# Optimization experiments

Hardware: AMD Instinct MI355X
Metric: run time of the kernel (lower is better)

## Reference

```python
import jax, jax.numpy as jnp
import numpy as np

SOBEL_X = jnp.array([[-1., 0., 1.], [-2., 0., 2.], [-1., 0., 1.]], dtype=jnp.float32).reshape(1, 1, 3, 3)
SOBEL_Y = jnp.array([[-1., -2., -1.], [0., 0., 0.], [1., 2., 1.]], dtype=jnp.float32).reshape(1, 1, 3, 3)


def _gray(x):
    # x: (B, 3, H, W) -> (B, 1, H, W)
    if x.shape[1] == 3:
        return 0.299 * x[:, 0:1] + 0.587 * x[:, 1:2] + 0.114 * x[:, 2:3]
    return x


def _edges(g):
    # g: (B, 1, H, W); 3x3 Sobel convs with padding 1 (cross-correlation, like torch conv2d)
    dn = ('NCHW', 'OIHW', 'NCHW')
    ex = jax.lax.conv_general_dilated(g, SOBEL_X, (1, 1), ((1, 1), (1, 1)), dimension_numbers=dn)
    ey = jax.lax.conv_general_dilated(g, SOBEL_Y, (1, 1), ((1, 1), (1, 1)), dimension_numbers=dn)
    return jnp.sqrt(ex * ex + ey * ey)


def setup_inputs() -> dict:
    key = jax.random.key(0)
    k1, k2 = jax.random.split(key)
    pred = jax.random.normal(k1, (32, 3, 512, 512), dtype=jnp.float32)
    target = jax.random.normal(k2, (32, 3, 512, 512), dtype=jnp.float32)
    return {"pred": pred, "target": target}


def reference(pred, target):
    pred_edges = _edges(_gray(pred))
    target_edges = _edges(_gray(target))
    return jnp.mean(jnp.abs(pred_edges - target_edges))
```

## Files before the change

### kernel.cpp

```cpp
#include <hip/hip_runtime.h>


#define BATCH 32
#define HH 512
#define WW 512
#define IMG ((size_t)HH * WW)
#define CHUNKS 128
#define TOTAL (BATCH * HH * CHUNKS)
#define GRID 2048

__global__ void zero_out_kernel(float* out) { out[0] = 0.0f; }

__device__ __forceinline__ float gray1(float r, float g, float b) {
    return 0.299f * r + 0.587f * g + 0.114f * b;
}

#define MAG(a0, a1, a2, b0, b2, c0, c1, c2)                              \
    ({ float ex_ = ((a2) - (a0)) + 2.0f * ((b2) - (b0)) + ((c2) - (c0)); \
       float ey_ = ((c0) - (a0)) + 2.0f * ((c1) - (a1)) + ((c2) - (a2)); \
       sqrtf(ex_ * ex_ + ey_ * ey_); })

__device__ __forceinline__ void edges4(const float* __restrict__ base,
                                       int row, int x0, bool okl, bool okr,
                                       float e[4])
{
    float g[3][6];
    #pragma unroll
    for (int k = 0; k < 3; ++k) {
        const int gy = row - 1 + k;
        if ((unsigned)gy < (unsigned)HH) {
            const float* rbase = base + (size_t)gy * WW;
            const float4 mr = *(const float4*)(rbase + x0);
            const float4 mg = *(const float4*)(rbase + IMG + x0);
            const float4 mb = *(const float4*)(rbase + 2 * IMG + x0);
            float lr = 0.f, lg = 0.f, lb = 0.f;
            float rr = 0.f, rg = 0.f, rb = 0.f;
            if (okl) {
                lr = rbase[x0 - 1];
                lg = rbase[IMG + x0 - 1];
                lb = rbase[2 * IMG + x0 - 1];
            }
            if (okr) {
                rr = rbase[x0 + 4];
                rg = rbase[IMG + x0 + 4];
                rb = rbase[2 * IMG + x0 + 4];
            }
            g[k][0] = gray1(lr, lg, lb);
            g[k][1] = gray1(mr.x, mg.x, mb.x);
            g[k][2] = gray1(mr.y, mg.y, mb.y);
            g[k][3] = gray1(mr.z, mg.z, mb.z);
            g[k][4] = gray1(mr.w, mg.w, mb.w);
            g[k][5] = gray1(rr, rg, rb);
        } else {
            #pragma unroll
            for (int i = 0; i < 6; ++i) g[k][i] = 0.f;
        }
    }
    #pragma unroll
    for (int j = 0; j < 4; ++j)
        e[j] = MAG(g[0][j], g[0][j + 1], g[0][j + 2],
                   g[1][j],             g[1][j + 2],
                   g[2][j], g[2][j + 1], g[2][j + 2]);
}

__global__ __launch_bounds__(256, 4) void edge_loss_kernel(
    const float* __restrict__ pred,
    const float* __restrict__ target,
    float* __restrict__ out)
{
    const int tid = threadIdx.x;
    float lsum = 0.0f;

    for (int idx = blockIdx.x * 256 + tid; idx < TOTAL; idx += GRID * 256) {
        const int img   = idx >> 16;
        const int row   = (idx >> 7) & 511;
        const int chunk = idx & 127;
        const int x0    = chunk << 2;
        const bool okl  = (chunk > 0);
        const bool okr  = (chunk < CHUNKS - 1);

        const float* pb = pred   + (size_t)img * 3 * IMG;
        const float* tb = target + (size_t)img * 3 * IMG;

        float ep[4], et[4];
        edges4(pb, row, x0, okl, okr, ep);
        edges4(tb, row, x0, okl, okr, et);

        lsum += fabsf(ep[0] - et[0]) + fabsf(ep[1] - et[1])
              + fabsf(ep[2] - et[2]) + fabsf(ep[3] - et[3]);
    }

    #pragma unroll
    for (int off = 32; off > 0; off >>= 1)
        lsum += __shfl_down(lsum, off, 64);

    __shared__ float wsum[4];
    const int lane = tid & 63;
    const int wav  = tid >> 6;
    if (lane == 0) wsum[wav] = lsum;
    __syncthreads();
    if (tid == 0) {
        const float s = wsum[0] + wsum[1] + wsum[2] + wsum[3];
        const float inv_n = 1.0f / ((float)BATCH * HH * WW);
        atomicAdd(out, s * inv_n);
    }
}

extern "C" void kernel_launch(void* const* d_in, const int* in_sizes, int n_in,
                              void* d_out, int out_size, void* d_ws, size_t ws_size,
                              hipStream_t stream) {
    const float* pred   = (const float*)d_in[0];
    const float* target = (const float*)d_in[1];
    float* out = (float*)d_out;

    zero_out_kernel<<<1, 1, 0, stream>>>(out);

    edge_loss_kernel<<<dim3(GRID, 1, 1), 256, 0, stream>>>(pred, target, out);
}
```

Before: 268.9 us.

## Use row-per-wave sliding window with lane shuffles for Sobel halos

```diff
diff --git a/kernel.cpp b/kernel.cpp
--- a/kernel.cpp
+++ b/kernel.cpp
@@ -5,104 +5,131 @@
 #define HH 512
 #define WW 512
 #define IMG ((size_t)HH * WW)
-#define CHUNKS 128
-#define TOTAL (BATCH * HH * CHUNKS)
-#define GRID 2048
 
 __global__ void zero_out_kernel(float* out) { out[0] = 0.0f; }
-
-__device__ __forceinline__ float gray1(float r, float g, float b) {
-    return 0.299f * r + 0.587f * g + 0.114f * b;
-}
 
 #define MAG(a0, a1, a2, b0, b2, c0, c1, c2)                              \
     ({ float ex_ = ((a2) - (a0)) + 2.0f * ((b2) - (b0)) + ((c2) - (c0)); \
        float ey_ = ((c0) - (a0)) + 2.0f * ((c1) - (a1)) + ((c2) - (a2)); \
        sqrtf(ex_ * ex_ + ey_ * ey_); })
 
-__device__ __forceinline__ void edges4(const float* __restrict__ base,
-                                       int row, int x0, bool okl, bool okr,
-                                       float e[4])
-{
-    float g[3][6];
-    #pragma unroll
-    for (int k = 0; k < 3; ++k) {
-        const int gy = row - 1 + k;
-        if ((unsigned)gy < (unsigned)HH) {
-            const float* rbase = base + (size_t)gy * WW;
-            const float4 mr = *(const float4*)(rbase + x0);
-            const float4 mg = *(const float4*)(rbase + IMG + x0);
-            const float4 mb = *(const float4*)(rbase + 2 * IMG + x0);
-            float lr = 0.f, lg = 0.f, lb = 0.f;
-            float rr = 0.f, rg = 0.f, rb = 0.f;
-            if (okl) {
-                lr = rbase[x0 - 1];
-                lg = rbase[IMG + x0 - 1];
-                lb = rbase[2 * IMG + x0 - 1];
-            }
-            if (okr) {
-                rr = rbase[x0 + 4];
-                rg = rbase[IMG + x0 + 4];
-                rb = rbase[2 * IMG + x0 + 4];
-            }
-            g[k][0] = gray1(lr, lg, lb);
-            g[k][1] = gray1(mr.x, mg.x, mb.x);
-            g[k][2] = gray1(mr.y, mg.y, mb.y);
-            g[k][3] = gray1(mr.z, mg.z, mb.z);
-            g[k][4] = gray1(mr.w, mg.w, mb.w);
-            g[k][5] = gray1(rr, rg, rb);
-        } else {
-            #pragma unroll
-            for (int i = 0; i < 6; ++i) g[k][i] = 0.f;
-        }
-    }
-    #pragma unroll
-    for (int j = 0; j < 4; ++j)
-        e[j] = MAG(g[0][j], g[0][j + 1], g[0][j + 2],
-                   g[1][j],             g[1][j + 2],
-                   g[2][j], g[2][j + 1], g[2][j + 2]);
-}
+#define LG(R, gy_) do {                                                   \
+    const int gy__ = (gy_);                                               \
+    if ((unsigned)gy__ < (unsigned)HH) {                                  \
+        const float* rp__ = pb + (size_t)gy__ * WW + cx;                  \
+        float4 x0_ = *(const float4*)(rp__);                              \
+        float4 x1_ = *(const float4*)(rp__ + 4);                          \
+        float4 y0_ = *(const float4*)(rp__ + IMG);                        \
+        float4 y1_ = *(const float4*)(rp__ + IMG + 4);                    \
+        float4 z0_ = *(const float4*)(rp__ + 2 * IMG);                    \
+        float4 z1_ = *(const float4*)(rp__ + 2 * IMG + 4);                \
+        R##p0 = 0.299f * x0_.x + 0.587f * y0_.x + 0.114f * z0_.x;         \
+        R##p1 = 0.299f * x0_.y + 0.587f * y0_.y + 0.114f * z0_.y;         \
+        R##p2 = 0.299f * x0_.z + 0.587f * y0_.z + 0.114f * z0_.z;         \
+        R##p3 = 0.299f * x0_.w + 0.587f * y0_.w + 0.114f * z0_.w;         \
+        R##p4 = 0.299f * x1_.x + 0.587f * y1_.x + 0.114f * z1_.x;         \
+        R##p5 = 0.299f * x1_.y + 0.587f * y1_.y + 0.114f * z1_.y;         \
+        R##p6 = 0.299f * x1_.z + 0.587f * y1_.z + 0.114f * z1_.z;         \
+        R##p7 = 0.299f * x1_.w + 0.587f * y1_.w + 0.114f * z1_.w;         \
+        const float* rt__ = tb + (size_t)gy__ * WW + cx;                  \
+        x0_ = *(const float4*)(rt__);                                     \
+        x1_ = *(const float4*)(rt__ + 4);                                 \
+        y0_ = *(const float4*)(rt__ + IMG);                               \
+        y1_ = *(const float4*)(rt__ + IMG + 4);                           \
+        z0_ = *(const float4*)(rt__ + 2 * IMG);                           \
+        z1_ = *(const float4*)(rt__ + 2 * IMG + 4);                       \
+        R##t0 = 0.299f * x0_.x + 0.587f * y0_.x + 0.114f * z0_.x;         \
+        R##t1 = 0.299f * x0_.y + 0.587f * y0_.y + 0.114f * z0_.y;         \
+        R##t2 = 0.299f * x0_.z + 0.587f * y0_.z + 0.114f * z0_.z;         \
+        R##t3 = 0.299f * x0_.w + 0.587f * y0_.w + 0.114f * z0_.w;         \
+        R##t4 = 0.299f * x1_.x + 0.587f * y1_.x + 0.114f * z1_.x;         \
+        R##t5 = 0.299f * x1_.y + 0.587f * y1_.y + 0.114f * z1_.y;         \
+        R##t6 = 0.299f * x1_.z + 0.587f * y1_.z + 0.114f * z1_.z;         \
+        R##t7 = 0.299f * x1_.w + 0.587f * y1_.w + 0.114f * z1_.w;         \
+    } else {                                                              \
+        R##p0 = R##p1 = R##p2 = R##p3 = 0.f;                              \
+        R##p4 = R##p5 = R##p6 = R##p7 = 0.f;                              \
+        R##t0 = R##t1 = R##t2 = R##t3 = 0.f;                              \
+        R##t4 = R##t5 = R##t6 = R##t7 = 0.f;                              \
+    }                                                                     \
+    { float s_;                                                           \
+      s_ = __shfl_up(R##p7, 1, 64);   R##pl = (lane == 0)  ? 0.f : s_;    \
+      s_ = __shfl_down(R##p0, 1, 64); R##pr = (lane == 63) ? 0.f : s_;    \
+      s_ = __shfl_up(R##t7, 1, 64);   R##tl = (lane == 0)  ? 0.f : s_;    \
+      s_ = __shfl_down(R##t0, 1, 64); R##tr = (lane == 63) ? 0.f : s_; }  \
+} while (0)
+
+#define SOB(A_, B_, C_) do {                                                        \
+    float ep_, et_;                                                                 \
+    ep_ = MAG(A_##pl, A_##p0, A_##p1,  B_##pl, B_##p1,  C_##pl, C_##p0, C_##p1);    \
+    et_ = MAG(A_##tl, A_##t0, A_##t1,  B_##tl, B_##t1,  C_##tl, C_##t0, C_##t1);    \
+    lsum += fabsf(ep_ - et_);                                                       \
+    ep_ = MAG(A_##p0, A_##p1, A_##p2,  B_##p0, B_##p2,  C_##p0, C_##p1, C_##p2);    \
+    et_ = MAG(A_##t0, A_##t1, A_##t2,  B_##t0, B_##t2,  C_##t0, C_##t1, C_##t2);    \
+    lsum += fabsf(ep_ - et_);                                                       \
+    ep_ = MAG(A_##p1, A_##p2, A_##p3,  B_##p1, B_##p3,  C_##p1, C_##p2, C_##p3);    \
+    et_ = MAG(A_##t1, A_##t2, A_##t3,  B_##t1, B_##t3,  C_##t1, C_##t2, C_##t3);    \
+    lsum += fabsf(ep_ - et_);                                                       \
+    ep_ = MAG(A_##p2, A_##p3, A_##p4,  B_##p2, B_##p4,  C_##p2, C_##p3, C_##p4);    \
+    et_ = MAG(A_##t2, A_##t3, A_##t4,  B_##t2, B_##t4,  C_##t2, C_##t3, C_##t4);    \
+    lsum += fabsf(ep_ - et_);                                                       \
+    ep_ = MAG(A_##p3, A_##p4, A_##p5,  B_##p3, B_##p5,  C_##p3, C_##p4, C_##p5);    \
+    et_ = MAG(A_##t3, A_##t4, A_##t5,  B_##t3, B_##t5,  C_##t3, C_##t4, C_##t5);    \
+    lsum += fabsf(ep_ - et_);                                                       \
+    ep_ = MAG(A_##p4, A_##p5, A_##p6,  B_##p4, B_##p6,  C_##p4, C_##p5, C_##p6);    \
+    et_ = MAG(A_##t4, A_##t5, A_##t6,  B_##t4, B_##t6,  C_##t4, C_##t5, C_##t6);    \
+    lsum += fabsf(ep_ - et_);                                                       \
+    ep_ = MAG(A_##p5, A_##p6, A_##p7,  B_##p5, B_##p7,  C_##p5, C_##p6, C_##p7);    \
+    et_ = MAG(A_##t5, A_##t6, A_##t7,  B_##t5, B_##t7,  C_##t5, C_##t6, C_##t7);    \
+    lsum += fabsf(ep_ - et_);                                                       \
+    ep_ = MAG(A_##p6, A_##p7, A_##pr,  B_##p6, B_##pr,  C_##p6, C_##p7, C_##pr);    \
+    et_ = MAG(A_##t6, A_##t7, A_##tr,  B_##t6, B_##tr,  C_##t6, C_##t7, C_##tr);    \
+    lsum += fabsf(ep_ - et_);                                                       \
+} while (0)
 
 __global__ __launch_bounds__(256, 4) void edge_loss_kernel(
     const float* __restrict__ pred,
     const float* __restrict__ target,
     float* __restrict__ out)
 {
-    const int tid = threadIdx.x;
+    const int tid  = threadIdx.x;
+    const int lane = tid & 63;
+    const int wav  = tid >> 6;
+    const int quad = blockIdx.x * 4 + wav;
+    const int img  = blockIdx.y;
+    const int y0   = quad * 4;
+    const int cx   = lane * 8;
+
+    const float* pb = pred   + (size_t)img * 3 * IMG;
+    const float* tb = target + (size_t)img * 3 * IMG;
+
+    float Ap0,Ap1,Ap2,Ap3,Ap4,Ap5,Ap6,Ap7, Apl,Apr;
+    float At0,At1,At2,At3,At4,At5,At6,At7, Atl,Atr;
+    float Bp0,Bp1,Bp2,Bp3,Bp4,Bp5,Bp6,Bp7, Bpl,Bpr;
+    float Bt0,Bt1,Bt2,Bt3,Bt4,Bt5,Bt6,Bt7, Btl,Btr;
+    float Cp0,Cp1,Cp2,Cp3,Cp4,Cp5,Cp6,Cp7, Cpl,Cpr;
+    float Ct0,Ct1,Ct2,Ct3,Ct4,Ct5,Ct6,Ct7, Ctl,Ctr;
+
     float lsum = 0.0f;
 
-    for (int idx = blockIdx.x * 256 + tid; idx < TOTAL; idx += GRID * 256) {
-        const int img   = idx >> 16;
-        const int row   = (idx >> 7) & 511;
-        const int chunk = idx & 127;
-        const int x0    = chunk << 2;
-        const bool okl  = (chunk > 0);
-        const bool okr  = (chunk < CHUNKS - 1);
-
-        const float* pb = pred   + (size_t)img * 3 * IMG;
-        const float* tb = target + (size_t)img * 3 * IMG;
-
-        float ep[4], et[4];
-        edges4(pb, row, x0, okl, okr, ep);
-        edges4(tb, row, x0, okl, okr, et);
-
-        lsum += fabsf(ep[0] - et[0]) + fabsf(ep[1] - et[1])
-              + fabsf(ep[2] - et[2]) + fabsf(ep[3] - et[3]);
-    }
+    LG(A, y0 - 1);
+    LG(B, y0);
+    LG(C, y0 + 1);
+    SOB(A, B, C);
+    LG(A, y0 + 2);
+    SOB(B, C, A);
+    LG(B, y0 + 3);
+    SOB(C, A, B);
+    LG(C, y0 + 4);
+    SOB(A, B, C);
 
     #pragma unroll
     for (int off = 32; off > 0; off >>= 1)
         lsum += __shfl_down(lsum, off, 64);
 
-    __shared__ float wsum[4];
-    const int lane = tid & 63;
-    const int wav  = tid >> 6;
-    if (lane == 0) wsum[wav] = lsum;
-    __syncthreads();
-    if (tid == 0) {
-        const float s = wsum[0] + wsum[1] + wsum[2] + wsum[3];
+    if (lane == 0) {
         const float inv_n = 1.0f / ((float)BATCH * HH * WW);
-        atomicAdd(out, s * inv_n);
+        atomicAdd(out, lsum * inv_n);
     }
 }
 
@@ -115,5 +142,6 @@
 
     zero_out_kernel<<<1, 1, 0, stream>>>(out);
 
-    edge_loss_kernel<<<dim3(GRID, 1, 1), 256, 0, stream>>>(pred, target, out);
+    dim3 grid(32, BATCH, 1);
+    edge_loss_kernel<<<grid, 256, 0, stream>>>(pred, target, out);
 }
```

After: 274.7 us. 2.2% more time.
